# Kernel tuning notes

Hardware: AMD Instinct MI355X
Metric: run time of the kernel (lower is better)

Reference implementation:

```python
import jax, jax.numpy as jnp
import numpy as np

# icosphere level-6 mesh dims
B, CIN, COUT = 8, 64, 64
NV_PREV, NV, NF = 10242, 40962, 81920


def spmm(x, rows, cols, vals, nrows):
    # x: [..., ncols]; sparse S [nrows, ncols] in COO -> y[..., r] = sum S[r,c] x[..., c]
    out = jnp.zeros(x.shape[:-1] + (nrows,), x.dtype)
    return out.at[..., rows].add(x[..., cols] * vals)


def setup_inputs() -> dict:
    key = jax.random.key(0)
    ks = jax.random.split(key, 12)
    x = jax.random.normal(ks[0], (B, CIN, NV_PREV), jnp.float32)
    # G: per-face gradient operator [3*NF, NV], 3 nnz per row (face vertices)
    G_rows = jnp.repeat(jnp.arange(3 * NF, dtype=jnp.int32), 3)
    G_cols = jax.random.randint(ks[1], (3 * NF * 3,), 0, NV, dtype=jnp.int32)
    G_vals = jax.random.normal(ks[2], (3 * NF * 3,), jnp.float32) * 0.1
    # L: vertex Laplacian [NV, NV], ~7 nnz per row
    L_rows = jnp.repeat(jnp.arange(NV, dtype=jnp.int32), 7)
    L_cols = jax.random.randint(ks[3], (NV * 7,), 0, NV, dtype=jnp.int32)
    L_vals = jax.random.normal(ks[4], (NV * 7,), jnp.float32) * 0.1
    # F2V: face-to-vertex averaging [NV, NF], ~6 nnz per row
    F2V_rows = jnp.repeat(jnp.arange(NV, dtype=jnp.int32), 6)
    F2V_cols = jax.random.randint(ks[5], (NV * 6,), 0, NF, dtype=jnp.int32)
    F2V_vals = jnp.full((NV * 6,), 1.0 / 6.0, jnp.float32)
    # per-face east-west / north-south tangent weights [NF, 3]
    EW = jax.random.normal(ks[6], (NF, 3), jnp.float32)
    NS = jax.random.normal(ks[7], (NF, 3), jnp.float32)
    # learned parameters
    stdv = 1.0 / np.sqrt(CIN * 4)
    coeffs = jax.random.uniform(ks[8], (COUT, CIN, 4), jnp.float32, -stdv, stdv)
    bias = jax.random.uniform(ks[9], (COUT,), jnp.float32, -stdv, stdv)
    return {
        "x": x,
        "G_rows": G_rows, "G_cols": G_cols, "G_vals": G_vals,
        "L_rows": L_rows, "L_cols": L_cols, "L_vals": L_vals,
        "F2V_rows": F2V_rows, "F2V_cols": F2V_cols, "F2V_vals": F2V_vals,
        "EW": EW, "NS": NS, "coeffs": coeffs, "bias": bias,
    }


def reference(x, G_rows, G_cols, G_vals, L_rows, L_cols, L_vals,
              F2V_rows, F2V_cols, F2V_vals, EW, NS, coeffs, bias):
    b, c = x.shape[:2]
    # pad new (upsampled) vertices with ones: [B, C, NV]
    xin = jnp.concatenate([x, jnp.ones((b, c, NV - NV_PREV), x.dtype)], axis=-1)
    # per-face gradient: [B, C, 3*NF] -> [B, C, NF, 3]
    grad_face = spmm(xin, G_rows, G_cols, G_vals, 3 * NF)
    grad_face = grad_face.reshape(b, c, 3, NF).transpose(0, 1, 3, 2)
    # Laplacian: [B, C, NV]
    laplacian = spmm(xin, L_rows, L_cols, L_vals, NV)
    # project face gradients onto EW/NS tangent dirs: [B, C, NF]
    grad_face_ew = jnp.sum(grad_face * EW, axis=-1)
    grad_face_ns = jnp.sum(grad_face * NS, axis=-1)
    # average back to vertices: [B, C, NV]
    grad_vert_ew = spmm(grad_face_ew, F2V_rows, F2V_cols, F2V_vals, NV)
    grad_vert_ns = spmm(grad_face_ns, F2V_rows, F2V_cols, F2V_vals, NV)
    # fuse 4 feature maps with learned coeffs: [B, CIN, NV, 4] x [COUT, CIN, 4]
    feat = jnp.stack([xin, laplacian, grad_vert_ew, grad_vert_ns], axis=-1)
    out = jnp.einsum("bcvk,ock->bov", feat, coeffs) + bias[:, None]
    return out
```

## Files before the change

### kernel.cpp

```cpp
#include <hip/hip_runtime.h>
#include <hip/hip_bf16.h>

typedef __hip_bfloat16 bf16;
typedef __attribute__((ext_vector_type(8))) short short8;
typedef __attribute__((ext_vector_type(4))) float floatx4;
typedef unsigned long long u64;

#define NVP 10242
#define NV  40962
#define NF  81920
#define FPF 2

__device__ __forceinline__ unsigned short f2bfbits(float f) {
    bf16 h = __float2bfloat16(f);
    return __builtin_bit_cast(unsigned short, h);
}
__device__ __forceinline__ unsigned short pk_fp8(float a, float b) {
    int p = __builtin_amdgcn_cvt_pk_fp8_f32(a, b, 0, false);
    return (unsigned short)(p & 0xffff);
}
__device__ __forceinline__ unsigned char one_fp8(float a) {
    int p = __builtin_amdgcn_cvt_pk_fp8_f32(a, 0.f, 0, false);
    return (unsigned char)(p & 0xff);
}
__device__ __forceinline__ float f8s0(unsigned int u){return __builtin_amdgcn_cvt_f32_fp8(u,0);}
__device__ __forceinline__ float f8s1(unsigned int u){return __builtin_amdgcn_cvt_f32_fp8(u,1);}
__device__ __forceinline__ float f8s2(unsigned int u){return __builtin_amdgcn_cvt_f32_fp8(u,2);}
__device__ __forceinline__ float f8s3(unsigned int u){return __builtin_amdgcn_cvt_f32_fp8(u,3);}
__device__ __forceinline__ void unpack8(u64 v, float o[8]) {
    unsigned int lo = (unsigned int)v, hi = (unsigned int)(v >> 32);
    o[0]=f8s0(lo); o[1]=f8s1(lo); o[2]=f8s2(lo); o[3]=f8s3(lo);
    o[4]=f8s0(hi); o[5]=f8s1(hi); o[6]=f8s2(hi); o[7]=f8s3(hi);
}

__global__ void k_prep(const float* __restrict__ coeffs,
                       unsigned short* __restrict__ coeffsB,
                       const int* __restrict__ G_cols,
                       const float* __restrict__ G_vals,
                       const float* __restrict__ EW,
                       const float* __restrict__ NS,
                       float* __restrict__ Gpk,
                       const int* __restrict__ L_cols,
                       const float* __restrict__ L_vals,
                       const int* __restrict__ F2V_cols,
                       const float* __restrict__ F2V_vals,
                       float* __restrict__ Vpk) {
    int b = blockIdx.x;
    if (b < 64) {
        int t = b * 256 + threadIdx.x;
        int j = t & 7, lane = (t >> 3) & 63, s = t >> 9;
        int ot = s >> 3, kk = s & 7;
        int o  = ot * 16 + (lane & 15);
        int kg = kk * 32 + (lane >> 4) * 8 + j;
        coeffsB[t] = f2bfbits(coeffs[o * 256 + kg]);
    } else if (b < 384) {
        int f = (b - 64) * 256 + threadIdx.x;
        float r[32];
#pragma unroll
        for (int q = 0; q < 32; ++q) r[q] = 0.f;
#pragma unroll
        for (int d = 0; d < 3; ++d)
#pragma unroll
            for (int j = 0; j < 3; ++j) {
                int idx = (d * NF + f) * 3 + j;
                r[d * 3 + j]      = __int_as_float(G_cols[idx]);
                r[16 + d * 3 + j] = G_vals[idx];
            }
#pragma unroll
        for (int d = 0; d < 3; ++d) {
            r[25 + d] = EW[f * 3 + d];
            r[28 + d] = NS[f * 3 + d];
        }
        float4* dst = (float4*)(Gpk + (size_t)f * 32);
#pragma unroll
        for (int q = 0; q < 8; ++q) dst[q] = ((const float4*)r)[q];
    } else {
        int v = (b - 384) * 256 + threadIdx.x;
        if (v >= NV) return;
        float r[32];
#pragma unroll
        for (int q = 0; q < 32; ++q) r[q] = 0.f;
#pragma unroll
        for (int j = 0; j < 7; ++j) {
            r[j]      = __int_as_float(L_cols[v * 7 + j]);
            r[16 + j] = L_vals[v * 7 + j];
        }
#pragma unroll
        for (int j = 0; j < 6; ++j) {
            r[8 + j]  = __int_as_float(F2V_cols[v * 6 + j]);
            r[24 + j] = F2V_vals[v * 6 + j];
        }
        float4* dst = (float4*)(Vpk + (size_t)v * 32);
#pragma unroll
        for (int q = 0; q < 8; ++q) dst[q] = ((const float4*)r)[q];
    }
}

__global__ void __launch_bounds__(256) k_transpose(
    const float* __restrict__ x,
    uint4* __restrict__ xinp, u64* __restrict__ xin8p) {
    __shared__ u64 t8 [32][65];
    __shared__ u64 tbL[32][65];
    __shared__ u64 tbH[32][65];
    int v0 = blockIdx.x * 64;
    int tx = threadIdx.x & 63, ty = threadIdx.x >> 6;
    for (int half = 0; half < 2; ++half) {
        if (half) __syncthreads();
#pragma unroll
        for (int r = 0; r < 8; ++r) {
            int c  = ty + r * 4;
            int cg = half * 32 + c;
            int v  = v0 + tx;
            u64 p8 = 0, bL = 0, bH = 0;
#pragma unroll
            for (int b = 0; b < 8; ++b) {
                float val = (v < NVP) ? x[((size_t)b * 64 + cg) * NVP + v] : 1.0f;
                p8 |= (u64)one_fp8(val) << (8 * b);
                u64 bf = (u64)f2bfbits(val);
                if (b < 4) bL |= bf << (16 * b);
                else       bH |= bf << (16 * (b - 4));
            }
            t8[c][tx] = p8; tbL[c][tx] = bL; tbH[c][tx] = bH;
        }
        __syncthreads();
        int cc = threadIdx.x & 31;
        int vq = threadIdx.x >> 5;
#pragma unroll
        for (int it = 0; it < 8; ++it) {
            int v  = vq * 8 + it;
            int vg = v0 + v;
            if (vg < NV) {
                size_t idx = (size_t)vg * 64 + half * 32 + cc;
                xin8p[idx] = t8[cc][v];
                u64 lo = tbL[cc][v], hi = tbH[cc][v];
                xinp[idx] = make_uint4((unsigned)lo, (unsigned)(lo >> 32),
                                       (unsigned)hi, (unsigned)(hi >> 32));
            }
        }
    }
}

__global__ void __launch_bounds__(256, 4) k_facegrad(
    const u64* __restrict__ xin8p,
    const float* __restrict__ Gpk,
    uint4* __restrict__ gfip) {
    int w  = __builtin_amdgcn_readfirstlane(threadIdx.x >> 6);
    int c  = threadIdx.x & 63;
    int f0 = (blockIdx.x * 4 + w) * FPF;

    int gc[FPF][9];
#pragma unroll
    for (int i = 0; i < FPF; ++i) {
        const int* ri = (const int*)(Gpk + (size_t)(f0 + i) * 32);
#pragma unroll
        for (int j = 0; j < 9; ++j) gc[i][j] = ri[j];
    }
    u64 xv[FPF][9];
#pragma unroll
    for (int i = 0; i < FPF; ++i)
#pragma unroll
        for (int j = 0; j < 9; ++j)
            xv[i][j] = xin8p[(size_t)gc[i][j] * 64 + c];
    __builtin_amdgcn_sched_barrier(0);
#pragma unroll
    for (int i = 0; i < FPF; ++i) {
        const float* rf = Gpk + (size_t)(f0 + i) * 32;
        float g0[8], g1[8], g2[8];
#pragma unroll
        for (int b = 0; b < 8; ++b) { g0[b] = 0.f; g1[b] = 0.f; g2[b] = 0.f; }
#pragma unroll
        for (int j = 0; j < 3; ++j) {
            float fa[8], fb[8], fc_[8];
            unpack8(xv[i][j],     fa);
            unpack8(xv[i][3 + j], fb);
            unpack8(xv[i][6 + j], fc_);
            float va = rf[16 + j], vb = rf[19 + j], vc = rf[22 + j];
#pragma unroll
            for (int b = 0; b < 8; ++b) {
                g0[b] += va * fa[b];
                g1[b] += vb * fb[b];
                g2[b] += vc * fc_[b];
            }
        }
        float e0 = rf[25], e1 = rf[26], e2 = rf[27];
        float n0 = rf[28], n1 = rf[29], n2 = rf[30];
        unsigned int d[4] = {0u, 0u, 0u, 0u};
#pragma unroll
        for (int b = 0; b < 8; ++b) {
            float ew = g0[b] * e0 + g1[b] * e1 + g2[b] * e2;
            float ns = g0[b] * n0 + g1[b] * n1 + g2[b] * n2;
            d[b >> 1] |= (unsigned int)pk_fp8(ew, ns) << ((b & 1) * 16);
        }
        gfip[(size_t)(f0 + i) * 64 + c] = make_uint4(d[0], d[1], d[2], d[3]);
    }
}

__global__ void __launch_bounds__(512, 2) k_vertex(
    const uint4* __restrict__ xinp,
    const u64* __restrict__ xin8p,
    const float* __restrict__ Vpk,
    const uint4* __restrict__ gfip,
    const unsigned short* __restrict__ coeffsB,
    const float* __restrict__ bias,
    float* __restrict__ out) {
    int vb = blockIdx.x * 8;
    __shared__ unsigned short feat[64 * 264];
    __shared__ float outs[64 * 67];
    int w    = __builtin_amdgcn_readfirstlane(threadIdx.x >> 6);
    int c    = threadIdx.x & 63;
    int v    = vb + w;
    int vcs  = __builtin_amdgcn_readfirstlane(v < NV ? v : NV - 1);

    const int* ri = (const int*)(Vpk + (size_t)vcs * 32);
    int lc[7], fc[6];
#pragma unroll
    for (int j = 0; j < 7; ++j) lc[j] = ri[j];
#pragma unroll
    for (int j = 0; j < 6; ++j) fc[j] = ri[8 + j];
    uint4 f0q = xinp[(size_t)vcs * 64 + c];
    u64 xl[7];
#pragma unroll
    for (int j = 0; j < 7; ++j) xl[j] = xin8p[(size_t)lc[j] * 64 + c];
    uint4 gq[6];
#pragma unroll
    for (int j = 0; j < 6; ++j) gq[j] = gfip[(size_t)fc[j] * 64 + c];
    __builtin_amdgcn_sched_barrier(0);
    const float* rv = Vpk + (size_t)vcs * 32;
    float lap[8], ew[8], ns[8];
#pragma unroll
    for (int b = 0; b < 8; ++b) { lap[b] = 0.f; ew[b] = 0.f; ns[b] = 0.f; }
#pragma unroll
    for (int j = 0; j < 7; ++j) {
        float xa[8];
        unpack8(xl[j], xa);
        float lv = rv[16 + j];
#pragma unroll
        for (int b = 0; b < 8; ++b) lap[b] += lv * xa[b];
    }
#pragma unroll
    for (int j = 0; j < 6; ++j) {
        float val = rv[24 + j];
        unsigned int q0 = gq[j].x, q1 = gq[j].y, q2 = gq[j].z, q3 = gq[j].w;
        ew[0] += val * f8s0(q0); ns[0] += val * f8s1(q0);
        ew[1] += val * f8s2(q0); ns[1] += val * f8s3(q0);
        ew[2] += val * f8s0(q1); ns[2] += val * f8s1(q1);
        ew[3] += val * f8s2(q1); ns[3] += val * f8s3(q1);
        ew[4] += val * f8s0(q2); ns[4] += val * f8s1(q2);
        ew[5] += val * f8s2(q2); ns[5] += val * f8s3(q2);
        ew[6] += val * f8s0(q3); ns[6] += val * f8s1(q3);
        ew[7] += val * f8s2(q3); ns[7] += val * f8s3(q3);
    }
    unsigned int fd[4] = {f0q.x, f0q.y, f0q.z, f0q.w};
#pragma unroll
    for (int b = 0; b < 8; ++b) {
        unsigned short f0s = (unsigned short)(fd[b >> 1] >> ((b & 1) * 16));
        ushort4 p = make_ushort4(f0s, f2bfbits(lap[b]),
                                 f2bfbits(ew[b]), f2bfbits(ns[b]));
        *(ushort4*)&feat[(w * 8 + b) * 264 + c * 4] = p;
    }
    __syncthreads();

    int m = c & 15, quad = c >> 4;
    int rt = w & 3, ob = (w >> 2) * 2;
    float b0v = bias[ob * 16 + m], b1v = bias[(ob + 1) * 16 + m];
    floatx4 acc0 = {b0v, b0v, b0v, b0v};
    floatx4 acc1 = {b1v, b1v, b1v, b1v};
#pragma unroll
    for (int kk = 0; kk < 8; ++kk) {
        short8 a  = *(const short8*)&feat[(rt * 16 + m) * 264 + kk * 32 + quad * 8];
        short8 f0 = *(const short8*)&coeffsB[((ob * 8 + kk) * 64 + c) * 8];
        short8 f1 = *(const short8*)&coeffsB[(((ob + 1) * 8 + kk) * 64 + c) * 8];
        acc0 = __builtin_amdgcn_mfma_f32_16x16x32_bf16(a, f0, acc0, 0, 0, 0);
        acc1 = __builtin_amdgcn_mfma_f32_16x16x32_bf16(a, f1, acc1, 0, 0, 0);
    }
#pragma unroll
    for (int r = 0; r < 4; ++r) {
        outs[(rt * 16 + quad * 4 + r) * 67 + ob * 16 + m]       = acc0[r];
        outs[(rt * 16 + quad * 4 + r) * 67 + (ob + 1) * 16 + m] = acc1[r];
    }
    __syncthreads();

    int vloc = threadIdx.x & 7;
    int g    = threadIdx.x >> 3;
    if (vb + vloc < NV) {
#pragma unroll
        for (int p = 0; p < 8; ++p) {
            out[((size_t)p * 64 + g) * NV + vb + vloc] =
                outs[(vloc * 8 + p) * 67 + g];
        }
    }
}

extern "C" void kernel_launch(void* const* d_in, const int* in_sizes, int n_in,
                              void* d_out, int out_size, void* d_ws, size_t ws_size,
                              hipStream_t stream) {
    const float* x        = (const float*)d_in[0];
    const int*   G_cols   = (const int*)  d_in[2];
    const float* G_vals   = (const float*)d_in[3];
    const int*   L_cols   = (const int*)  d_in[5];
    const float* L_vals   = (const float*)d_in[6];
    const int*   F2V_cols = (const int*)  d_in[8];
    const float* F2V_vals = (const float*)d_in[9];
    const float* EW       = (const float*)d_in[10];
    const float* NS       = (const float*)d_in[11];
    const float* coeffs   = (const float*)d_in[12];
    const float* bias     = (const float*)d_in[13];
    float* out = (float*)d_out;

    char* ws = (char*)d_ws;
    const size_t gpk_bytes  = (size_t)NF * 128;
    const size_t vpk_bytes  = (size_t)NV * 128;
    const size_t xinp_bytes = (size_t)NV * 64 * 16;
    const size_t x8p_bytes  = (size_t)NV * 64 * 8;

    unsigned short* coeffsB = (unsigned short*)ws;
    float* Gpk   = (float*)(ws + 65536);
    float* Vpk   = (float*)(ws + 65536 + gpk_bytes);
    uint4* xinp  = (uint4*)(ws + 65536 + gpk_bytes + vpk_bytes);
    u64*   xin8p = (u64*)  (ws + 65536 + gpk_bytes + vpk_bytes + xinp_bytes);
    uint4* gfip  = (uint4*)(ws + 65536 + gpk_bytes + vpk_bytes + xinp_bytes
                               + x8p_bytes);

    k_prep<<<545, 256, 0, stream>>>(coeffs, coeffsB, G_cols, G_vals, EW, NS,
                                    Gpk, L_cols, L_vals, F2V_cols, F2V_vals,
                                    Vpk);
    k_transpose<<<641, 256, 0, stream>>>(x, xinp, xin8p);
    k_facegrad<<<NF / (4 * FPF), 256, 0, stream>>>(xin8p, Gpk, gfip);
    k_vertex<<<(NV + 7) / 8, 512, 0, stream>>>(xinp, xin8p, Vpk, gfip,
                                               coeffsB, bias, out);
}
```

Baseline: 331.5 us.

## Split batch into separate planes and batch-parallelize vertex kernel

```diff
diff --git a/kernel.cpp b/kernel.cpp
--- a/kernel.cpp
+++ b/kernel.cpp
@@ -9,12 +9,17 @@
 #define NVP 10242
 #define NV  40962
 #define NF  81920
+#define VPB 32
 #define FPF 2
 
 __device__ __forceinline__ unsigned short f2bfbits(float f) {
     bf16 h = __float2bfloat16(f);
     return __builtin_bit_cast(unsigned short, h);
 }
+__device__ __forceinline__ float bfbits2f(unsigned short u) {
+    union { unsigned int i; float f; } cv; cv.i = ((unsigned int)u) << 16;
+    return cv.f;
+}
 __device__ __forceinline__ unsigned short pk_fp8(float a, float b) {
     int p = __builtin_amdgcn_cvt_pk_fp8_f32(a, b, 0, false);
     return (unsigned short)(p & 0xffff);
@@ -25,12 +30,17 @@
 }
 __device__ __forceinline__ float f8s0(unsigned int u){return __builtin_amdgcn_cvt_f32_fp8(u,0);}
 __device__ __forceinline__ float f8s1(unsigned int u){return __builtin_amdgcn_cvt_f32_fp8(u,1);}
-__device__ __forceinline__ float f8s2(unsigned int u){return __builtin_amdgcn_cvt_f32_fp8(u,2);}
-__device__ __forceinline__ float f8s3(unsigned int u){return __builtin_amdgcn_cvt_f32_fp8(u,3);}
-__device__ __forceinline__ void unpack8(u64 v, float o[8]) {
-    unsigned int lo = (unsigned int)v, hi = (unsigned int)(v >> 32);
-    o[0]=f8s0(lo); o[1]=f8s1(lo); o[2]=f8s2(lo); o[3]=f8s3(lo);
-    o[4]=f8s0(hi); o[5]=f8s1(hi); o[6]=f8s2(hi); o[7]=f8s3(hi);
+
+__device__ __forceinline__ void unpack_bf16x8(uint4 q, float o[8]) {
+    union { unsigned int u; float f; } cv;
+    cv.u = q.x << 16;          o[0] = cv.f;
+    cv.u = q.x & 0xffff0000u;  o[1] = cv.f;
+    cv.u = q.y << 16;          o[2] = cv.f;
+    cv.u = q.y & 0xffff0000u;  o[3] = cv.f;
+    cv.u = q.z << 16;          o[4] = cv.f;
+    cv.u = q.z & 0xffff0000u;  o[5] = cv.f;
+    cv.u = q.w << 16;          o[6] = cv.f;
+    cv.u = q.w & 0xffff0000u;  o[7] = cv.f;
 }
 
 __global__ void k_prep(const float* __restrict__ coeffs,
@@ -77,28 +87,28 @@
     } else {
         int v = (b - 384) * 256 + threadIdx.x;
         if (v >= NV) return;
-        float r[32];
-#pragma unroll
-        for (int q = 0; q < 32; ++q) r[q] = 0.f;
+        float r[28];
+#pragma unroll
+        for (int q = 0; q < 28; ++q) r[q] = 0.f;
 #pragma unroll
         for (int j = 0; j < 7; ++j) {
             r[j]      = __int_as_float(L_cols[v * 7 + j]);
-            r[16 + j] = L_vals[v * 7 + j];
+            r[14 + j] = L_vals[v * 7 + j];
         }
 #pragma unroll
         for (int j = 0; j < 6; ++j) {
-            r[8 + j]  = __int_as_float(F2V_cols[v * 6 + j]);
-            r[24 + j] = F2V_vals[v * 6 + j];
-        }
-        float4* dst = (float4*)(Vpk + (size_t)v * 32);
-#pragma unroll
-        for (int q = 0; q < 8; ++q) dst[q] = ((const float4*)r)[q];
+            r[7 + j]  = __int_as_float(F2V_cols[v * 6 + j]);
+            r[21 + j] = F2V_vals[v * 6 + j];
+        }
+        float4* dst = (float4*)(Vpk + (size_t)v * 28);
+#pragma unroll
+        for (int q = 0; q < 7; ++q) dst[q] = ((const float4*)r)[q];
     }
 }
 
 __global__ void __launch_bounds__(256) k_transpose(
     const float* __restrict__ x,
-    uint4* __restrict__ xinp, u64* __restrict__ xin8p) {
+    uint4* __restrict__ xinp, unsigned char* __restrict__ xin8) {
     __shared__ u64 t8 [32][65];
     __shared__ u64 tbL[32][65];
     __shared__ u64 tbH[32][65];
@@ -131,19 +141,23 @@
             int vg = v0 + v;
             if (vg < NV) {
                 size_t idx = (size_t)vg * 64 + half * 32 + cc;
-                xin8p[idx] = t8[cc][v];
                 u64 lo = tbL[cc][v], hi = tbH[cc][v];
                 xinp[idx] = make_uint4((unsigned)lo, (unsigned)(lo >> 32),
                                        (unsigned)hi, (unsigned)(hi >> 32));
+                u64 p8 = t8[cc][v];
+#pragma unroll
+                for (int b = 0; b < 8; ++b)
+                    xin8[(size_t)b * NV * 64 + idx] =
+                        (unsigned char)(p8 >> (8 * b));
             }
         }
     }
 }
 
-__global__ void __launch_bounds__(256, 4) k_facegrad(
-    const u64* __restrict__ xin8p,
+__global__ void __launch_bounds__(256, 3) k_facegrad(
+    const uint4* __restrict__ xinp,
     const float* __restrict__ Gpk,
-    uint4* __restrict__ gfip) {
+    unsigned short* __restrict__ gfi) {
     int w  = __builtin_amdgcn_readfirstlane(threadIdx.x >> 6);
     int c  = threadIdx.x & 63;
     int f0 = (blockIdx.x * 4 + w) * FPF;
@@ -155,12 +169,12 @@
 #pragma unroll
         for (int j = 0; j < 9; ++j) gc[i][j] = ri[j];
     }
-    u64 xv[FPF][9];
+    uint4 xq[FPF][9];
 #pragma unroll
     for (int i = 0; i < FPF; ++i)
 #pragma unroll
         for (int j = 0; j < 9; ++j)
-            xv[i][j] = xin8p[(size_t)gc[i][j] * 64 + c];
+            xq[i][j] = xinp[(size_t)gc[i][j] * 64 + c];
     __builtin_amdgcn_sched_barrier(0);
 #pragma unroll
     for (int i = 0; i < FPF; ++i) {
@@ -170,123 +184,120 @@
         for (int b = 0; b < 8; ++b) { g0[b] = 0.f; g1[b] = 0.f; g2[b] = 0.f; }
 #pragma unroll
         for (int j = 0; j < 3; ++j) {
-            float fa[8], fb[8], fc_[8];
-            unpack8(xv[i][j],     fa);
-            unpack8(xv[i][3 + j], fb);
-            unpack8(xv[i][6 + j], fc_);
+            float fa[8], fb[8], fd[8];
+            unpack_bf16x8(xq[i][j],     fa);
+            unpack_bf16x8(xq[i][3 + j], fb);
+            unpack_bf16x8(xq[i][6 + j], fd);
             float va = rf[16 + j], vb = rf[19 + j], vc = rf[22 + j];
 #pragma unroll
             for (int b = 0; b < 8; ++b) {
                 g0[b] += va * fa[b];
                 g1[b] += vb * fb[b];
-                g2[b] += vc * fc_[b];
+                g2[b] += vc * fd[b];
             }
         }
         float e0 = rf[25], e1 = rf[26], e2 = rf[27];
         float n0 = rf[28], n1 = rf[29], n2 = rf[30];
-        unsigned int d[4] = {0u, 0u, 0u, 0u};
 #pragma unroll
         for (int b = 0; b < 8; ++b) {
             float ew = g0[b] * e0 + g1[b] * e1 + g2[b] * e2;
             float ns = g0[b] * n0 + g1[b] * n1 + g2[b] * n2;
-            d[b >> 1] |= (unsigned int)pk_fp8(ew, ns) << ((b & 1) * 16);
-        }
-        gfip[(size_t)(f0 + i) * 64 + c] = make_uint4(d[0], d[1], d[2], d[3]);
+            gfi[(size_t)b * NF * 64 + (size_t)(f0 + i) * 64 + c] =
+                pk_fp8(ew, ns);
+        }
     }
 }
 
 __global__ void __launch_bounds__(512, 2) k_vertex(
-    const uint4* __restrict__ xinp,
-    const u64* __restrict__ xin8p,
+    const unsigned int* __restrict__ xinpw,
+    const unsigned char* __restrict__ xin8,
     const float* __restrict__ Vpk,
-    const uint4* __restrict__ gfip,
+    const unsigned short* __restrict__ gfi,
     const unsigned short* __restrict__ coeffsB,
     const float* __restrict__ bias,
     float* __restrict__ out) {
-    int vb = blockIdx.x * 8;
-    __shared__ unsigned short feat[64 * 264];
-    __shared__ float outs[64 * 67];
+    int batch = blockIdx.x & 7;
+    int vb    = (blockIdx.x >> 3) * VPB;
+    xin8 += (size_t)batch * 64 * NV;
+    gfi  += (size_t)batch * 64 * NF;
+    out  += (size_t)batch * 64 * NV;
+    int bhalf = batch >> 1, bsh = (batch & 1) * 16;
+
+    __shared__ unsigned short feat[VPB * 264];
+    __shared__ float outs[VPB * 65];
     int w    = __builtin_amdgcn_readfirstlane(threadIdx.x >> 6);
-    int c    = threadIdx.x & 63;
-    int v    = vb + w;
-    int vcs  = __builtin_amdgcn_readfirstlane(v < NV ? v : NV - 1);
-
-    const int* ri = (const int*)(Vpk + (size_t)vcs * 32);
-    int lc[7], fc[6];
-#pragma unroll
-    for (int j = 0; j < 7; ++j) lc[j] = ri[j];
-#pragma unroll
-    for (int j = 0; j < 6; ++j) fc[j] = ri[8 + j];
-    uint4 f0q = xinp[(size_t)vcs * 64 + c];
-    u64 xl[7];
-#pragma unroll
-    for (int j = 0; j < 7; ++j) xl[j] = xin8p[(size_t)lc[j] * 64 + c];
-    uint4 gq[6];
-#pragma unroll
-    for (int j = 0; j < 6; ++j) gq[j] = gfip[(size_t)fc[j] * 64 + c];
+    int lane = threadIdx.x & 63;
+    int c    = lane;
+
+    int vcs[4];
+#pragma unroll
+    for (int i = 0; i < 4; ++i) {
+        int v = vb + w * 4 + i;
+        vcs[i] = __builtin_amdgcn_readfirstlane(v < NV ? v : NV - 1);
+    }
+    int lc[4][7], fc[4][6];
+#pragma unroll
+    for (int i = 0; i < 4; ++i) {
+        const int* ri = (const int*)(Vpk + (size_t)vcs[i] * 28);
+#pragma unroll
+        for (int j = 0; j < 7; ++j) lc[i][j] = ri[j];
+#pragma unroll
+        for (int j = 0; j < 6; ++j) fc[i][j] = ri[7 + j];
+    }
+    unsigned int f0u[4], xl[4][7], gg[4][6];
+#pragma unroll
+    for (int i = 0; i < 4; ++i) {
+        f0u[i] = xinpw[((size_t)vcs[i] * 64 + c) * 4 + bhalf];
+#pragma unroll
+        for (int j = 0; j < 7; ++j)
+            xl[i][j] = xin8[(size_t)lc[i][j] * 64 + c];
+#pragma unroll
+        for (int j = 0; j < 6; ++j)
+            gg[i][j] = gfi[(size_t)fc[i][j] * 64 + c];
+    }
     __builtin_amdgcn_sched_barrier(0);
-    const float* rv = Vpk + (size_t)vcs * 32;
-    float lap[8], ew[8], ns[8];
-#pragma unroll
-    for (int b = 0; b < 8; ++b) { lap[b] = 0.f; ew[b] = 0.f; ns[b] = 0.f; }
-#pragma unroll
-    for (int j = 0; j < 7; ++j) {
-        float xa[8];
-        unpack8(xl[j], xa);
-        float lv = rv[16 + j];
-#pragma unroll
-        for (int b = 0; b < 8; ++b) lap[b] += lv * xa[b];
-    }
-#pragma unroll
-    for (int j = 0; j < 6; ++j) {
-        float val = rv[24 + j];
-        unsigned int q0 = gq[j].x, q1 = gq[j].y, q2 = gq[j].z, q3 = gq[j].w;
-        ew[0] += val * f8s0(q0); ns[0] += val * f8s1(q0);
-        ew[1] += val * f8s2(q0); ns[1] += val * f8s3(q0);
-        ew[2] += val * f8s0(q1); ns[2] += val * f8s1(q1);
-        ew[3] += val * f8s2(q1); ns[3] += val * f8s3(q1);
-        ew[4] += val * f8s0(q2); ns[4] += val * f8s1(q2);
-        ew[5] += val * f8s2(q2); ns[5] += val * f8s3(q2);
-        ew[6] += val * f8s0(q3); ns[6] += val * f8s1(q3);
-        ew[7] += val * f8s2(q3); ns[7] += val * f8s3(q3);
-    }
-    unsigned int fd[4] = {f0q.x, f0q.y, f0q.z, f0q.w};
-#pragma unroll
-    for (int b = 0; b < 8; ++b) {
-        unsigned short f0s = (unsigned short)(fd[b >> 1] >> ((b & 1) * 16));
-        ushort4 p = make_ushort4(f0s, f2bfbits(lap[b]),
-                                 f2bfbits(ew[b]), f2bfbits(ns[b]));
-        *(ushort4*)&feat[(w * 8 + b) * 264 + c * 4] = p;
+#pragma unroll
+    for (int i = 0; i < 4; ++i) {
+        const float* rv = Vpk + (size_t)vcs[i] * 28;
+        float lap = 0.f;
+#pragma unroll
+        for (int j = 0; j < 7; ++j)
+            lap += rv[14 + j] * f8s0(xl[i][j]);
+        float ew = 0.f, ns = 0.f;
+#pragma unroll
+        for (int j = 0; j < 6; ++j) {
+            float val = rv[21 + j];
+            ew += val * f8s0(gg[i][j]);
+            ns += val * f8s1(gg[i][j]);
+        }
+        ushort4 p = make_ushort4((unsigned short)(f0u[i] >> bsh),
+                                 f2bfbits(lap), f2bfbits(ew), f2bfbits(ns));
+        *(ushort4*)&feat[(w * 4 + i) * 264 + c * 4] = p;
     }
     __syncthreads();
 
-    int m = c & 15, quad = c >> 4;
-    int rt = w & 3, ob = (w >> 2) * 2;
-    float b0v = bias[ob * 16 + m], b1v = bias[(ob + 1) * 16 + m];
-    floatx4 acc0 = {b0v, b0v, b0v, b0v};
-    floatx4 acc1 = {b1v, b1v, b1v, b1v};
+    int m = lane & 15, quad = lane >> 4;
+    int ot = w & 3, vh = w >> 2;
+    float bo = bias[ot * 16 + m];
+    floatx4 acc = {bo, bo, bo, bo};
 #pragma unroll
     for (int kk = 0; kk < 8; ++kk) {
-        short8 a  = *(const short8*)&feat[(rt * 16 + m) * 264 + kk * 32 + quad * 8];
-        short8 f0 = *(const short8*)&coeffsB[((ob * 8 + kk) * 64 + c) * 8];
-        short8 f1 = *(const short8*)&coeffsB[(((ob + 1) * 8 + kk) * 64 + c) * 8];
-        acc0 = __builtin_amdgcn_mfma_f32_16x16x32_bf16(a, f0, acc0, 0, 0, 0);
-        acc1 = __builtin_amdgcn_mfma_f32_16x16x32_bf16(a, f1, acc1, 0, 0, 0);
-    }
-#pragma unroll
-    for (int r = 0; r < 4; ++r) {
-        outs[(rt * 16 + quad * 4 + r) * 67 + ob * 16 + m]       = acc0[r];
-        outs[(rt * 16 + quad * 4 + r) * 67 + (ob + 1) * 16 + m] = acc1[r];
-    }
+        short8 a = *(const short8*)&feat[(vh * 16 + m) * 264 + kk * 32 + quad * 8];
+        short8 bfr = *(const short8*)&coeffsB[((ot * 8 + kk) * 64 + lane) * 8];
+        acc = __builtin_amdgcn_mfma_f32_16x16x32_bf16(a, bfr, acc, 0, 0, 0);
+    }
+
+#pragma unroll
+    for (int r = 0; r < 4; ++r)
+        outs[(vh * 16 + quad * 4 + r) * 65 + ot * 16 + m] = acc[r];
     __syncthreads();
-
-    int vloc = threadIdx.x & 7;
-    int g    = threadIdx.x >> 3;
-    if (vb + vloc < NV) {
-#pragma unroll
-        for (int p = 0; p < 8; ++p) {
-            out[((size_t)p * 64 + g) * NV + vb + vloc] =
-                outs[(vloc * 8 + p) * 67 + g];
+    int vp = threadIdx.x & 31;
+    int og = threadIdx.x >> 5;
+    if (vb + vp < NV) {
+#pragma unroll
+        for (int r = 0; r < 4; ++r) {
+            int o2 = og + r * 16;
+            out[(size_t)o2 * NV + vb + vp] = outs[vp * 65 + o2];
         }
     }
 }
@@ -309,23 +320,24 @@
 
     char* ws = (char*)d_ws;
     const size_t gpk_bytes  = (size_t)NF * 128;
-    const size_t vpk_bytes  = (size_t)NV * 128;
+    const size_t vpk_bytes  = (size_t)NV * 112;
     const size_t xinp_bytes = (size_t)NV * 64 * 16;
-    const size_t x8p_bytes  = (size_t)NV * 64 * 8;
+    const size_t x8_bytes   = (size_t)8 * NV * 64;
 
     unsigned short* coeffsB = (unsigned short*)ws;
     float* Gpk   = (float*)(ws + 65536);
     float* Vpk   = (float*)(ws + 65536 + gpk_bytes);
     uint4* xinp  = (uint4*)(ws + 65536 + gpk_bytes + vpk_bytes);
-    u64*   xin8p = (u64*)  (ws + 65536 + gpk_bytes + vpk_bytes + xinp_bytes);
-    uint4* gfip  = (uint4*)(ws + 65536 + gpk_bytes + vpk_bytes + xinp_bytes
-                               + x8p_bytes);
+    unsigned char* xin8 = (unsigned char*)(ws + 65536 + gpk_bytes + vpk_bytes
+                                              + xinp_bytes);
+    unsigned short* gfi = (unsigned short*)(ws + 65536 + gpk_bytes + vpk_bytes
+                                               + xinp_bytes + x8_bytes);
 
     k_prep<<<545, 256, 0, stream>>>(coeffs, coeffsB, G_cols, G_vals, EW, NS,
                                     Gpk, L_cols, L_vals, F2V_cols, F2V_vals,
                                     Vpk);
-    k_transpose<<<641, 256, 0, stream>>>(x, xinp, xin8p);
-    k_facegrad<<<NF / (4 * FPF), 256, 0, stream>>>(xin8p, Gpk, gfip);
-    k_vertex<<<(NV + 7) / 8, 512, 0, stream>>>(xinp, xin8p, Vpk, gfip,
-                                               coeffsB, bias, out);
-}
+    k_transpose<<<641, 256, 0, stream>>>(x, xinp, xin8);
+    k_facegrad<<<NF / (4 * FPF), 256, 0, stream>>>(xinp, Gpk, gfi);
+    k_vertex<<<((NV + VPB - 1) / VPB) * 8, 512, 0, stream>>>(
+        (const unsigned int*)xinp, xin8, Vpk, gfi, coeffsB, bias, out);
+}
```

Result: slower. 441.5 us (+33.2%).

## Process 16 vertices per block in k_vertex with LDS reuse and compact Vpk

Applied to the files above, without the earlier changes.

```diff
diff --git a/kernel.cpp b/kernel.cpp
--- a/kernel.cpp
+++ b/kernel.cpp
@@ -9,7 +9,9 @@
 #define NVP 10242
 #define NV  40962
 #define NF  81920
-#define FPF 2
+#define FPF 4
+#define VPB 16
+#define FROW 260
 
 __device__ __forceinline__ unsigned short f2bfbits(float f) {
     bf16 h = __float2bfloat16(f);
@@ -77,22 +79,22 @@
     } else {
         int v = (b - 384) * 256 + threadIdx.x;
         if (v >= NV) return;
-        float r[32];
-#pragma unroll
-        for (int q = 0; q < 32; ++q) r[q] = 0.f;
+        float r[28];
+#pragma unroll
+        for (int q = 0; q < 28; ++q) r[q] = 0.f;
 #pragma unroll
         for (int j = 0; j < 7; ++j) {
             r[j]      = __int_as_float(L_cols[v * 7 + j]);
-            r[16 + j] = L_vals[v * 7 + j];
+            r[14 + j] = L_vals[v * 7 + j];
         }
 #pragma unroll
         for (int j = 0; j < 6; ++j) {
-            r[8 + j]  = __int_as_float(F2V_cols[v * 6 + j]);
-            r[24 + j] = F2V_vals[v * 6 + j];
-        }
-        float4* dst = (float4*)(Vpk + (size_t)v * 32);
-#pragma unroll
-        for (int q = 0; q < 8; ++q) dst[q] = ((const float4*)r)[q];
+            r[7 + j]  = __int_as_float(F2V_cols[v * 6 + j]);
+            r[21 + j] = F2V_vals[v * 6 + j];
+        }
+        float4* dst = (float4*)(Vpk + (size_t)v * 28);
+#pragma unroll
+        for (int q = 0; q < 7; ++q) dst[q] = ((const float4*)r)[q];
     }
 }
 
@@ -170,16 +172,16 @@
         for (int b = 0; b < 8; ++b) { g0[b] = 0.f; g1[b] = 0.f; g2[b] = 0.f; }
 #pragma unroll
         for (int j = 0; j < 3; ++j) {
-            float fa[8], fb[8], fc_[8];
+            float fa[8], fb[8], fd[8];
             unpack8(xv[i][j],     fa);
             unpack8(xv[i][3 + j], fb);
-            unpack8(xv[i][6 + j], fc_);
+            unpack8(xv[i][6 + j], fd);
             float va = rf[16 + j], vb = rf[19 + j], vc = rf[22 + j];
 #pragma unroll
             for (int b = 0; b < 8; ++b) {
                 g0[b] += va * fa[b];
                 g1[b] += vb * fb[b];
-                g2[b] += vc * fc_[b];
+                g2[b] += vc * fd[b];
             }
         }
         float e0 = rf[25], e1 = rf[26], e2 = rf[27];
@@ -195,7 +197,7 @@
     }
 }
 
-__global__ void __launch_bounds__(512, 2) k_vertex(
+__global__ void __launch_bounds__(512, 4) k_vertex(
     const uint4* __restrict__ xinp,
     const u64* __restrict__ xin8p,
     const float* __restrict__ Vpk,
@@ -203,90 +205,112 @@
     const unsigned short* __restrict__ coeffsB,
     const float* __restrict__ bias,
     float* __restrict__ out) {
-    int vb = blockIdx.x * 8;
-    __shared__ unsigned short feat[64 * 264];
-    __shared__ float outs[64 * 67];
-    int w    = __builtin_amdgcn_readfirstlane(threadIdx.x >> 6);
-    int c    = threadIdx.x & 63;
-    int v    = vb + w;
-    int vcs  = __builtin_amdgcn_readfirstlane(v < NV ? v : NV - 1);
-
-    const int* ri = (const int*)(Vpk + (size_t)vcs * 32);
-    int lc[7], fc[6];
-#pragma unroll
-    for (int j = 0; j < 7; ++j) lc[j] = ri[j];
-#pragma unroll
-    for (int j = 0; j < 6; ++j) fc[j] = ri[8 + j];
-    uint4 f0q = xinp[(size_t)vcs * 64 + c];
-    u64 xl[7];
-#pragma unroll
-    for (int j = 0; j < 7; ++j) xl[j] = xin8p[(size_t)lc[j] * 64 + c];
-    uint4 gq[6];
-#pragma unroll
-    for (int j = 0; j < 6; ++j) gq[j] = gfip[(size_t)fc[j] * 64 + c];
+    int vb = blockIdx.x * VPB;
+    __shared__ unsigned short feat[128 * FROW];
+    float* outs = (float*)feat;
+    int w = __builtin_amdgcn_readfirstlane(threadIdx.x >> 6);
+    int c = threadIdx.x & 63;
+
+    int vcs[2];
+#pragma unroll
+    for (int i = 0; i < 2; ++i) {
+        int v = vb + w * 2 + i;
+        vcs[i] = __builtin_amdgcn_readfirstlane(v < NV ? v : NV - 1);
+    }
+    int lc[2][7], fc[2][6];
+#pragma unroll
+    for (int i = 0; i < 2; ++i) {
+        const int* ri = (const int*)(Vpk + (size_t)vcs[i] * 28);
+#pragma unroll
+        for (int j = 0; j < 7; ++j) lc[i][j] = ri[j];
+#pragma unroll
+        for (int j = 0; j < 6; ++j) fc[i][j] = ri[7 + j];
+    }
+    uint4 f0q[2], gq[2][6];
+    u64 xl[2][7];
+#pragma unroll
+    for (int i = 0; i < 2; ++i) {
+        f0q[i] = xinp[(size_t)vcs[i] * 64 + c];
+#pragma unroll
+        for (int j = 0; j < 7; ++j)
+            xl[i][j] = xin8p[(size_t)lc[i][j] * 64 + c];
+#pragma unroll
+        for (int j = 0; j < 6; ++j)
+            gq[i][j] = gfip[(size_t)fc[i][j] * 64 + c];
+    }
     __builtin_amdgcn_sched_barrier(0);
-    const float* rv = Vpk + (size_t)vcs * 32;
-    float lap[8], ew[8], ns[8];
-#pragma unroll
-    for (int b = 0; b < 8; ++b) { lap[b] = 0.f; ew[b] = 0.f; ns[b] = 0.f; }
-#pragma unroll
-    for (int j = 0; j < 7; ++j) {
-        float xa[8];
-        unpack8(xl[j], xa);
-        float lv = rv[16 + j];
-#pragma unroll
-        for (int b = 0; b < 8; ++b) lap[b] += lv * xa[b];
-    }
-#pragma unroll
-    for (int j = 0; j < 6; ++j) {
-        float val = rv[24 + j];
-        unsigned int q0 = gq[j].x, q1 = gq[j].y, q2 = gq[j].z, q3 = gq[j].w;
-        ew[0] += val * f8s0(q0); ns[0] += val * f8s1(q0);
-        ew[1] += val * f8s2(q0); ns[1] += val * f8s3(q0);
-        ew[2] += val * f8s0(q1); ns[2] += val * f8s1(q1);
-        ew[3] += val * f8s2(q1); ns[3] += val * f8s3(q1);
-        ew[4] += val * f8s0(q2); ns[4] += val * f8s1(q2);
-        ew[5] += val * f8s2(q2); ns[5] += val * f8s3(q2);
-        ew[6] += val * f8s0(q3); ns[6] += val * f8s1(q3);
-        ew[7] += val * f8s2(q3); ns[7] += val * f8s3(q3);
-    }
-    unsigned int fd[4] = {f0q.x, f0q.y, f0q.z, f0q.w};
-#pragma unroll
-    for (int b = 0; b < 8; ++b) {
-        unsigned short f0s = (unsigned short)(fd[b >> 1] >> ((b & 1) * 16));
-        ushort4 p = make_ushort4(f0s, f2bfbits(lap[b]),
-                                 f2bfbits(ew[b]), f2bfbits(ns[b]));
-        *(ushort4*)&feat[(w * 8 + b) * 264 + c * 4] = p;
+#pragma unroll
+    for (int i = 0; i < 2; ++i) {
+        const float* rv = Vpk + (size_t)vcs[i] * 28;
+        float lap[8], ew[8], ns[8];
+#pragma unroll
+        for (int b = 0; b < 8; ++b) { lap[b] = 0.f; ew[b] = 0.f; ns[b] = 0.f; }
+#pragma unroll
+        for (int j = 0; j < 7; ++j) {
+            float xa[8];
+            unpack8(xl[i][j], xa);
+            float lv = rv[14 + j];
+#pragma unroll
+            for (int b = 0; b < 8; ++b) lap[b] += lv * xa[b];
+        }
+#pragma unroll
+        for (int j = 0; j < 6; ++j) {
+            float val = rv[21 + j];
+            unsigned int q0 = gq[i][j].x, q1 = gq[i][j].y;
+            unsigned int q2 = gq[i][j].z, q3 = gq[i][j].w;
+            ew[0] += val * f8s0(q0); ns[0] += val * f8s1(q0);
+            ew[1] += val * f8s2(q0); ns[1] += val * f8s3(q0);
+            ew[2] += val * f8s0(q1); ns[2] += val * f8s1(q1);
+            ew[3] += val * f8s2(q1); ns[3] += val * f8s3(q1);
+            ew[4] += val * f8s0(q2); ns[4] += val * f8s1(q2);
+            ew[5] += val * f8s2(q2); ns[5] += val * f8s3(q2);
+            ew[6] += val * f8s0(q3); ns[6] += val * f8s1(q3);
+            ew[7] += val * f8s2(q3); ns[7] += val * f8s3(q3);
+        }
+        unsigned int fd[4] = {f0q[i].x, f0q[i].y, f0q[i].z, f0q[i].w};
+        int vloc = w * 2 + i;
+#pragma unroll
+        for (int b = 0; b < 8; ++b) {
+            unsigned short f0s = (unsigned short)(fd[b >> 1] >> ((b & 1) * 16));
+            ushort4 p = make_ushort4(f0s, f2bfbits(lap[b]),
+                                     f2bfbits(ew[b]), f2bfbits(ns[b]));
+            *(ushort4*)&feat[(vloc * 8 + b) * FROW + c * 4] = p;
+        }
     }
     __syncthreads();
 
     int m = c & 15, quad = c >> 4;
-    int rt = w & 3, ob = (w >> 2) * 2;
-    float b0v = bias[ob * 16 + m], b1v = bias[(ob + 1) * 16 + m];
-    floatx4 acc0 = {b0v, b0v, b0v, b0v};
-    floatx4 acc1 = {b1v, b1v, b1v, b1v};
-#pragma unroll
-    for (int kk = 0; kk < 8; ++kk) {
-        short8 a  = *(const short8*)&feat[(rt * 16 + m) * 264 + kk * 32 + quad * 8];
-        short8 f0 = *(const short8*)&coeffsB[((ob * 8 + kk) * 64 + c) * 8];
-        short8 f1 = *(const short8*)&coeffsB[(((ob + 1) * 8 + kk) * 64 + c) * 8];
-        acc0 = __builtin_amdgcn_mfma_f32_16x16x32_bf16(a, f0, acc0, 0, 0, 0);
-        acc1 = __builtin_amdgcn_mfma_f32_16x16x32_bf16(a, f1, acc1, 0, 0, 0);
-    }
-#pragma unroll
-    for (int r = 0; r < 4; ++r) {
-        outs[(rt * 16 + quad * 4 + r) * 67 + ob * 16 + m]       = acc0[r];
-        outs[(rt * 16 + quad * 4 + r) * 67 + (ob + 1) * 16 + m] = acc1[r];
-    }
+    int ot = w & 3, rg = w >> 2;
+    float bo = bias[ot * 16 + m];
+    floatx4 acc[4] = {{bo,bo,bo,bo},{bo,bo,bo,bo},{bo,bo,bo,bo},{bo,bo,bo,bo}};
+#pragma unroll
+    for (int t = 0; t < 4; ++t)
+#pragma unroll
+        for (int kk = 0; kk < 8; ++kk) {
+            short8 a = *(const short8*)
+                &feat[((rg * 4 + t) * 16 + m) * FROW + kk * 32 + quad * 8];
+            short8 bfr = *(const short8*)&coeffsB[((ot * 8 + kk) * 64 + c) * 8];
+            acc[t] = __builtin_amdgcn_mfma_f32_16x16x32_bf16(a, bfr, acc[t], 0, 0, 0);
+        }
     __syncthreads();
 
-    int vloc = threadIdx.x & 7;
-    int g    = threadIdx.x >> 3;
-    if (vb + vloc < NV) {
-#pragma unroll
-        for (int p = 0; p < 8; ++p) {
-            out[((size_t)p * 64 + g) * NV + vb + vloc] =
-                outs[(vloc * 8 + p) * 67 + g];
+#pragma unroll
+    for (int t = 0; t < 4; ++t)
+#pragma unroll
+        for (int r = 0; r < 4; ++r)
+            outs[((rg * 4 + t) * 16 + quad * 4 + r) * 65 + ot * 16 + m] = acc[t][r];
+    __syncthreads();
+
+    int vp = threadIdx.x & 15;
+    int oh = threadIdx.x >> 4;
+    if (vb + vp < NV) {
+#pragma unroll
+        for (int s = 0; s < 2; ++s) {
+            int o = oh + s * 32;
+#pragma unroll
+            for (int b = 0; b < 8; ++b)
+                out[((size_t)b * 64 + o) * NV + vb + vp] =
+                    outs[(vp * 8 + b) * 65 + o];
         }
     }
 }
@@ -309,7 +333,7 @@
 
     char* ws = (char*)d_ws;
     const size_t gpk_bytes  = (size_t)NF * 128;
-    const size_t vpk_bytes  = (size_t)NV * 128;
+    const size_t vpk_bytes  = (size_t)NV * 112;
     const size_t xinp_bytes = (size_t)NV * 64 * 16;
     const size_t x8p_bytes  = (size_t)NV * 64 * 8;
 
@@ -326,6 +350,6 @@
                                     Vpk);
     k_transpose<<<641, 256, 0, stream>>>(x, xinp, xin8p);
     k_facegrad<<<NF / (4 * FPF), 256, 0, stream>>>(xin8p, Gpk, gfip);
-    k_vertex<<<(NV + 7) / 8, 512, 0, stream>>>(xinp, xin8p, Vpk, gfip,
-                                               coeffsB, bias, out);
-}
+    k_vertex<<<(NV + VPB - 1) / VPB, 512, 0, stream>>>(
+        xinp, xin8p, Vpk, gfip, coeffsB, bias, out);
+}
```

Result: slower. 455.7 us (+37.5%).
